# Kernel optimization log

Hardware: AMD Instinct MI355X
Metric: run time of the kernel (lower is better)

## Reference

```python
import jax, jax.numpy as jnp
import numpy as np

B, T, N, D = 32, 12, 325, 64
H = 4           # geo_num_heads == t_num_heads
HD = D // H     # head_dim = 16
M_SP = 32       # spatial frequency modes (min(32, N//2))
M_T = T // 2    # temporal frequency modes (all low modes)
SCALE = HD ** -0.5


def _lin(x, W):
    # torch nn.Linear (no bias): y = x @ W.T, W: [out, in]
    return jnp.einsum('btnd,ed->btne', x, W)


def _spatial(x, Wq, Wk, Wv, weights_Q, sp_modes):
    # FEDformer-style frequency attention over the node axis N
    q, k, v = _lin(x, Wq), _lin(x, Wk), _lin(x, Wv)          # [B,T,N,D]
    prep = lambda y: y.reshape(B, T, N, H, HD).transpose(0, 1, 3, 4, 2)  # [B,T,H,HD,N]
    qn = prep(q) / jnp.linalg.norm(q)   # global Frobenius norm (torch.norm with no dim)
    kn = prep(k) / jnp.linalg.norm(k)
    vn = prep(v)
    # rfft over nodes, gather selected modes (scatter-into-zeros in torch == gather here
    # since target indices are 0..M-1)
    qf = jnp.fft.rfft(qn, axis=-1)[..., sp_modes]            # [B,T,H,HD,M] c64
    kf = jnp.fft.rfft(kn, axis=-1)[..., sp_modes]
    vf = jnp.fft.rfft(vn, axis=-1)[..., sp_modes]
    M = M_SP
    qg = qf.transpose(0, 1, 2, 4, 3)[:, :, :, :, None, :]    # [B,T,H,M,1,HD]
    wq = jnp.broadcast_to(weights_Q.astype(jnp.complex64), (B, T, H, M, M - 1, HD))
    q_cat = jnp.concatenate([qg, wq], axis=4)                # [B,T,H,M,M,HD]
    kg = kf.transpose(0, 1, 2, 4, 3)[:, :, :, None, :, :]    # [B,T,H,1,M,HD]
    att = kg * jnp.conj(q_cat) * SCALE                       # [B,T,H,M,M,HD] c64
    att = jax.nn.softmax(jnp.abs(att), axis=-2).astype(jnp.complex64)
    att = att.transpose(0, 1, 2, 3, 5, 4)                    # [B,T,H,M,HD,M]
    vg = vf[:, :, :, None, :, :]                             # [B,T,H,1,HD,M]
    out = (vg * jnp.conj(att)).mean(axis=3)                  # [B,T,H,HD,M]
    out_ft = jnp.zeros((B, T, H, HD, N // 2 + 1), jnp.complex64).at[..., sp_modes].set(out)
    y = jnp.fft.irfft(out_ft, n=N, axis=-1)                  # [B,T,H,HD,N]
    return y.transpose(0, 1, 4, 2, 3).reshape(B, T, N, D)


def _temporal(x, Wq, Wk, Wv, weights_Q_t, t_modes):
    # frequency attention over the time axis T with causal (tril) mask.
    # NOTE: torch reshapes the [B,T,N,D] buffer directly as [B,N,T,H,HD] (raw view),
    # so we replicate that exact buffer reinterpretation.
    q, k, v = _lin(x, Wq), _lin(x, Wk), _lin(x, Wv)
    prep = lambda y: y.reshape(B, N, T, H, HD).transpose(0, 1, 3, 4, 2)  # [B,N,H,HD,T]
    qn = prep(q); kn = prep(k); vn = prep(v)
    qn = qn / jnp.linalg.norm(qn)
    kn = kn / jnp.linalg.norm(kn)
    qf = jnp.fft.rfft(qn, axis=-1)[..., t_modes]             # [B,N,H,HD,Mt]
    kf = jnp.fft.rfft(kn, axis=-1)[..., t_modes]
    vf = jnp.fft.rfft(vn, axis=-1)[..., t_modes]
    Mt = M_T
    qg = qf.transpose(0, 1, 2, 4, 3)[:, :, :, :, None, :]    # [B,N,H,Mt,1,HD]
    wq = jnp.broadcast_to(weights_Q_t.astype(jnp.complex64), (B, N, H, Mt, Mt - 1, HD))
    q_cat = jnp.concatenate([qg, wq], axis=4)                # [B,N,H,Mt,Mt,HD]
    kg = kf.transpose(0, 1, 2, 4, 3)[:, :, :, :, None, :]    # [B,N,H,Mt,1,HD] (unsqueeze(4) in torch)
    att = kg * jnp.conj(q_cat) * SCALE                       # [B,N,H,Mt,Mt,HD]
    att = att.transpose(0, 1, 2, 5, 3, 4)                    # [B,N,H,HD,Mt,Mt]
    mask = jnp.tril(jnp.ones((Mt, Mt), jnp.float32))
    att = att * mask                                         # zero above diagonal
    attw = jax.nn.softmax(jnp.abs(att), axis=-1).astype(jnp.complex64)
    vg = vf[..., None]                                       # [B,N,H,HD,Mt,1]
    out = (vg * jnp.conj(attw)).mean(axis=-1)                # [B,N,H,HD,Mt]
    out_ft = jnp.zeros((B, N, H, HD, T // 2 + 1), jnp.complex64).at[..., t_modes].set(out)
    y = jnp.fft.irfft(out_ft, n=T, axis=-1)                  # [B,N,H,HD,T]
    return y.transpose(0, 4, 1, 2, 3).reshape(B, T, N, D)


def _gcn(x, adj, W_fc1, W_mlp, b_mlp):
    a = adj / jnp.sum(adj, axis=1, keepdims=True)            # row-normalized
    agg = jnp.einsum('btkd,nk->btnd', x, a)
    h = jnp.einsum('btnd,ed->btne', agg, W_fc1)              # fc1 (no bias)
    return jnp.einsum('btnd,ed->btne', h, W_mlp) + b_mlp     # mlp (bias)


def _forward(x, adj, Wq_geo, Wk_geo, Wv_geo, Wq_t, Wk_t, Wv_t,
             W_fc1, W_mlp, b_mlp, weights_Q, weights_Q_t, sp_modes, t_modes):
    gcn_out = _gcn(x, adj, W_fc1, W_mlp, b_mlp)
    sp_x = _spatial(x, Wq_geo, Wk_geo, Wv_geo, weights_Q, sp_modes)
    te_x = _temporal(x, Wq_t, Wk_t, Wv_t, weights_Q_t, t_modes)
    return gcn_out + sp_x + te_x   # proj_drop is identity (p=0)


def setup_inputs() -> dict:
    key = jax.random.key(0)
    ks = jax.random.split(key, 13)
    w = lambda k, s: jax.random.normal(k, s, dtype=jnp.float32) * 0.05
    rng = np.random.default_rng(0)
    sp_modes = np.sort(rng.permutation(N // 2)[:M_SP]).astype(np.int32)
    t_modes = np.arange(M_T, dtype=np.int32)  # modes_T == T//2 selects all low modes
    return {
        'x': jax.random.normal(ks[0], (B, T, N, D), dtype=jnp.float32),
        'adj': jax.random.uniform(ks[1], (N, N), dtype=jnp.float32),
        'Wq_geo': w(ks[2], (D, D)), 'Wk_geo': w(ks[3], (D, D)), 'Wv_geo': w(ks[4], (D, D)),
        'Wq_t': w(ks[5], (D, D)), 'Wk_t': w(ks[6], (D, D)), 'Wv_t': w(ks[7], (D, D)),
        'W_fc1': w(ks[8], (D, D)), 'W_mlp': w(ks[9], (D, D)), 'b_mlp': w(ks[10], (D,)),
        'weights_Q': jax.random.normal(ks[11], (M_SP, M_SP - 1, HD), dtype=jnp.float32),
        'weights_Q_t': jax.random.normal(ks[12], (M_T, M_T - 1, HD), dtype=jnp.float32),
        'sp_modes': jnp.asarray(sp_modes),
        't_modes': jnp.asarray(t_modes),
    }


def reference(x, adj, Wq_geo, Wk_geo, Wv_geo, Wq_t, Wk_t, Wv_t,
              W_fc1, W_mlp, b_mlp, weights_Q, weights_Q_t, sp_modes, t_modes):
    return _forward(x, adj, Wq_geo, Wk_geo, Wv_geo, Wq_t, Wk_t, Wv_t,
                    W_fc1, W_mlp, b_mlp, weights_Q, weights_Q_t, sp_modes, t_modes)
```

## Files before the change

kernel.cpp:

```cpp
#include <hip/hip_runtime.h>


typedef unsigned short u16;
typedef short short8 __attribute__((ext_vector_type(8)));
typedef float floatx4 __attribute__((ext_vector_type(4)));

__device__ __forceinline__ u16 f2bf(float f) {
  union { float fp; unsigned int u; } v; v.fp = f;
  unsigned int x = v.u;
  x += 0x7FFF + ((x >> 16) & 1);
  return (u16)(x >> 16);
}

constexpr size_t OFF_NORM = 4096;
constexpr size_t OFF_WQA  = 8208;
constexpr size_t OFF_ANB  = 24080;
constexpr size_t OFF_TB   = 81280;
constexpr size_t OFF_T2   = 102080;
constexpr size_t OFF_OFT  = 112480;
constexpr size_t OFF_XCT  = 898912;
constexpr size_t OFF_WBB  = 5224288;
constexpr size_t OFF_WSPB = 5226336;
constexpr size_t OFF_WVTB = 5232480;
constexpr size_t OFF_XA   = 13211488;

__global__ __launch_bounds__(256) void k_prep(const float* __restrict__ x,
                                              const float* __restrict__ Wmlp,
                                              const float* __restrict__ Wfc1,
                                              const float* __restrict__ wQ,
                                              const float* __restrict__ Wq,
                                              const float* __restrict__ Wk,
                                              const float* __restrict__ Wv,
                                              const int* __restrict__ sp_modes,
                                              float* __restrict__ ws) {
  __shared__ float red[256];
  __shared__ __align__(16) u16 XA[128 * 72];
  const int tid = threadIdx.x;
  const int blk = blockIdx.x;
  u16* WBBu = (u16*)(ws + OFF_WBB);
  if (blk >= 22) {
    const int blk2 = blk - 22;
    const int wv = tid >> 6, lane = tid & 63, lc = lane & 15, quad = lane >> 4;
    const size_t base = (size_t)blk2 * 128;
    for (int i = tid; i < 2048; i += 256) {
      const int row = i >> 4, e0 = (i & 15) * 4;
      const float4 v = *(const float4*)(x + (base + row) * 64 + e0);
      u16* dst = &XA[row * 72 + e0];
      dst[0] = f2bf(v.x); dst[1] = f2bf(v.y); dst[2] = f2bf(v.z); dst[3] = f2bf(v.w);
    }
    __syncthreads();
    floatx4 acc[2][8] = {};
#pragma unroll
    for (int kc = 0; kc < 2; ++kc) {
      short8 af[2];
#pragma unroll
      for (int mi = 0; mi < 2; ++mi)
        af[mi] = *(const short8*)&XA[(32 * wv + 16 * mi + lc) * 72 + kc * 32 + quad * 8];
#pragma unroll
      for (int ni = 0; ni < 8; ++ni) {
        const int g = (ni & 3) * 16 + lc;
        const float* src = ((ni < 4) ? Wq : Wk) + (size_t)g * 64 + kc * 32 + quad * 8;
        float v8[8];
        *(float4*)v8 = *(const float4*)src;
        *(float4*)(v8 + 4) = *(const float4*)(src + 4);
        short8 bf_;
#pragma unroll
        for (int u = 0; u < 8; ++u) bf_[u] = (short)f2bf(v8[u]);
#pragma unroll
        for (int mi = 0; mi < 2; ++mi)
          acc[mi][ni] = __builtin_amdgcn_mfma_f32_16x16x32_bf16(af[mi], bf_, acc[mi][ni], 0, 0, 0);
      }
    }
    float sq = 0.f, sk = 0.f;
#pragma unroll
    for (int mi = 0; mi < 2; ++mi)
#pragma unroll
      for (int reg = 0; reg < 4; ++reg) {
#pragma unroll
        for (int ni = 0; ni < 4; ++ni) {
          const float v = acc[mi][ni][reg];
          sq = fmaf(v, v, sq);
        }
#pragma unroll
        for (int ni = 4; ni < 8; ++ni) {
          const float v = acc[mi][ni][reg];
          sk = fmaf(v, v, sk);
        }
      }
    for (int off = 32; off > 0; off >>= 1) {
      sq += __shfl_down(sq, off);
      sk += __shfl_down(sk, off);
    }
    if (lane == 0) { red[wv] = sq; red[8 + wv] = sk; }
    __syncthreads();
    if (tid == 0) {
      const size_t bucket = OFF_NORM + 32 * (size_t)(blk2 & 15);
      atomicAdd(&ws[bucket + 0], red[0] + red[1] + red[2] + red[3]);
      atomicAdd(&ws[bucket + 1], red[8] + red[9] + red[10] + red[11]);
    }
    return;
  }
  if (blk == 0) {
    for (int o = tid; o < 4096; o += 256) {
      int g = o >> 6, dd = o & 63;
      float s = 0.f;
      for (int e = 0; e < 64; ++e)
        s = fmaf(Wmlp[g * 64 + e], Wfc1[e * 64 + dd], s);
      WBBu[o] = f2bf(s);
    }
  } else if (blk < 9) {
    for (int i = (blk - 1) * 256 + tid; i < 15872; i += 2048)
      ws[OFF_WQA + i] = fabsf(wQ[i]);
  } else if (blk < 21) {
    const int j = blk - 9;
    u16* T2B = (u16*)(ws + OFF_T2);
    u16* TB = (u16*)(ws + OFF_TB);
    for (int jj = j; jj < 32; jj += 12) {
      const int f = sp_modes[jj];
      const float wgt = (f == 0) ? 1.f : 2.f;
      const int row_re = 8 * (jj >> 2) + (jj & 3);
      const int row_im = row_re + 4;
      for (int n = tid; n < 352; n += 256) {
        float c = 0.f, s = 0.f;
        if (n < 325) {
          int mm = (f * n) % 325;
          float th = 6.283185307179586f * (float)mm * (1.f / 325.f);
          c = cosf(th);
          s = sinf(th);
        }
        TB[(size_t)row_re * 352 + n] = f2bf(c);
        TB[(size_t)row_im * 352 + n] = f2bf(-s);
        if (n < 325) {
          T2B[(size_t)n * 64 + 2 * jj] = f2bf(wgt * (1.f / 325.f) * c);
          T2B[(size_t)n * 64 + 2 * jj + 1] = f2bf(-wgt * (1.f / 325.f) * s);
        }
      }
    }
  } else {
    u16* WSPBu = (u16*)(ws + OFF_WSPB);
    for (int i = tid; i < 12288; i += 256) {
      const int r = i >> 6, e = i & 63;
      const float* src = (r < 64) ? Wq : (r < 128) ? Wk : Wv;
      WSPBu[i] = f2bf(src[(size_t)(r & 63) * 64 + e]);
    }
  }
}

__global__ __launch_bounds__(256) void k_mega(const float* __restrict__ x,
                                              const float* __restrict__ adj,
                                              const float* __restrict__ Wvt,
                                              float* __restrict__ ws) {
  __shared__ __align__(16) float smem[12800];
  const int tid = threadIdx.x;
  const int blk = blockIdx.x;
  const int lane = tid & 63, wv = tid >> 6;
  const int lc = lane & 15, quad = lane >> 4;

  if (blk < 384) {
    const int bt = blk;
    u16* XBu = (u16*)smem;
    float g_nq = 0.f, g_nk = 0.f;
#pragma unroll
    for (int k2 = 0; k2 < 16; ++k2) {
      const float2 v = *(const float2*)(ws + OFF_NORM + 32 * (size_t)k2);
      g_nq += v.x; g_nk += v.y;
    }

    const u16* TB = (const u16*)(ws + OFF_TB);
    const u16* WSPBu = (const u16*)(ws + OFF_WSPB);
    const float* xb = x + (size_t)bt * 20800;
    const int br = tid & 31, be0 = (tid >> 5) * 8;

    {
      float va[4][8];
#pragma unroll
      for (int g = 0; g < 3; ++g) {
        const int nkc = (g < 2) ? 4 : 3;
#pragma unroll
        for (int u = 0; u < 4; ++u) {
          if (u >= nkc) break;
          const int k0 = (g * 4 + u) * 32;
          if (k0 + br < 325) {
            const float* src = xb + (size_t)(k0 + br) * 64 + be0;
            *(float4*)&va[u][0] = *(const float4*)src;
            *(float4*)&va[u][4] = *(const float4*)(src + 4);
          } else {
#pragma unroll
            for (int w = 0; w < 8; ++w) va[u][w] = 0.f;
          }
        }
#pragma unroll
        for (int u = 0; u < 4; ++u) {
          if (u >= nkc) break;
          const int k0 = (g * 4 + u) * 32;
#pragma unroll
          for (int w = 0; w < 8; ++w)
            XBu[(be0 + w) * 360 + k0 + br] = f2bf(va[u][w]);
        }
      }
    }
    __syncthreads();

    floatx4 accA[4] = {};
#pragma unroll
    for (int kc = 0; kc < 11; ++kc) {
      const short8 af = *(const short8*)&TB[(size_t)(16 * wv + lc) * 352 + kc * 32 + quad * 8];
#pragma unroll
      for (int t = 0; t < 4; ++t) {
        const short8 bf_ = *(const short8*)&XBu[(t * 16 + lc) * 360 + kc * 32 + quad * 8];
        accA[t] = __builtin_amdgcn_mfma_f32_16x16x32_bf16(af, bf_, accA[t], 0, 0, 0);
      }
    }
    __syncthreads();

    u16* xfl2 = XBu;
#pragma unroll
    for (int t = 0; t < 4; ++t)
#pragma unroll
      for (int r = 0; r < 4; ++r)
        xfl2[(t >> 1) * 2560 + (16 * wv + quad * 4 + r) * 40 + (t & 1) * 16 + lc] =
            f2bf(accA[t][r]);
    __syncthreads();

    floatx4 acc2[12] = {};
#pragma unroll
    for (int kc2 = 0; kc2 < 2; ++kc2) {
      const short8 af2 = *(const short8*)&xfl2[kc2 * 2560 + (16 * wv + lc) * 40 + quad * 8];
#pragma unroll
      for (int t = 0; t < 12; ++t) {
        const short8 bf2 = *(const short8*)&WSPBu[(t * 16 + lc) * 64 + kc2 * 32 + quad * 8];
        acc2[t] = __builtin_amdgcn_mfma_f32_16x16x32_bf16(af2, bf2, acc2[t], 0, 0, 0);
      }
    }
    __syncthreads();

    float* sq_q = smem + 2560;
    float* sq_k = smem + 4608;
    float* vfre = smem + 6656;
    float* vfim = smem + 8704;
    float* wbar = smem + 10752;
    for (int i = tid; i < 2048; i += 256) wbar[i] = 0.f;
    {
      const int fb = 8 * wv + ((quad >= 2) ? 4 : 0);
      const int isim = quad & 1;
#pragma unroll
      for (int t = 0; t < 12; ++t) {
        const int mat = t >> 2;
        const int d = (t & 3) * 16 + lc;
#pragma unroll
        for (int r = 0; r < 4; ++r) {
          const float v = acc2[t][r];
          if (mat == 2) {
            if (isim) vfim[(fb + r) * 64 + d] = v;
            else vfre[(fb + r) * 64 + d] = v;
          } else {
            const float s2 = v * v + __shfl_xor(v * v, 16);
            if (!isim) {
              if (mat == 0) sq_q[(fb + r) * 64 + d] = s2;
              else sq_k[(fb + r) * 64 + d] = s2;
            }
          }
        }
      }
    }
    __syncthreads();
    const float inv_nq = rsqrtf(g_nq);
    const float inv_nk = rsqrtf(g_nk);
    for (int i = tid; i < 2048; i += 256)
      sq_k[i] = 0.25f * inv_nk * sqrtf(sq_k[i]);
    __syncthreads();
    {
      const int d = tid & 63, fb2 = tid >> 6, hd = d & 15;
      const float* wqa = ws + OFF_WQA;
      float wacc[32];
#pragma unroll
      for (int j = 0; j < 32; ++j) wacc[j] = 0.f;
      for (int r8 = 0; r8 < 8; ++r8) {
        const int m = fb2 + (r8 << 2);
        const float aq = inv_nq * sqrtf(sq_q[m * 64 + d]);
        float sv[32];
        float mx = -1e30f;
#pragma unroll
        for (int j = 0; j < 32; ++j) {
          const float a = (j == 0) ? aq : wqa[(m * 31 + (j - 1)) * 16 + hd];
          const float s = sq_k[j * 64 + d] * a;
          sv[j] = s;
          mx = fmaxf(mx, s);
        }
        float sum = 0.f;
#pragma unroll
        for (int j = 0; j < 32; ++j) {
          const float ev = __expf(sv[j] - mx);
          sv[j] = ev;
          sum += ev;
        }
        const float sc = 0.03125f / sum;
#pragma unroll
        for (int j = 0; j < 32; ++j) wacc[j] += sv[j] * sc;
      }
#pragma unroll
      for (int j = 0; j < 32; ++j) atomicAdd(&wbar[j * 64 + d], wacc[j]);
    }
    __syncthreads();
    unsigned int* OFTu = (unsigned int*)(ws + OFF_OFT) + (size_t)bt * 2048;
    for (int i2 = tid; i2 < 2048; i2 += 256) {
      const int d = i2 >> 5, j = i2 & 31;
      const float w = wbar[j * 64 + d];
      const unsigned int lo = f2bf(vfre[j * 64 + d] * w);
      const unsigned int hi = f2bf(vfim[j * 64 + d] * w);
      OFTu[i2] = lo | (hi << 16);
    }
  } else if (blk < 1359) {
    const int blk2 = blk - 384;
    u16* XAu = (u16*)smem;
    const size_t base = (size_t)blk2 * 128;
    const u16* WBBu = (const u16*)(ws + OFF_WBB);

    for (int i = tid; i < 2048; i += 256) {
      const int row = i >> 4, e0 = (i & 15) * 4;
      const float4 v = *(const float4*)(x + (base + row) * 64 + e0);
      u16* dst = &XAu[row * 72 + e0];
      dst[0] = f2bf(v.x); dst[1] = f2bf(v.y); dst[2] = f2bf(v.z); dst[3] = f2bf(v.w);
    }
    __syncthreads();

    floatx4 acc[2][4] = {};
#pragma unroll
    for (int kc = 0; kc < 2; ++kc) {
      short8 af[2];
#pragma unroll
      for (int mi = 0; mi < 2; ++mi)
        af[mi] = *(const short8*)&XAu[(32 * wv + 16 * mi + lc) * 72 + kc * 32 + quad * 8];
#pragma unroll
      for (int ni = 0; ni < 4; ++ni) {
        const short8 bf_ = *(const short8*)&WBBu[(ni * 16 + lc) * 64 + kc * 32 + quad * 8];
#pragma unroll
        for (int mi = 0; mi < 2; ++mi)
          acc[mi][ni] = __builtin_amdgcn_mfma_f32_16x16x32_bf16(af[mi], bf_, acc[mi][ni], 0, 0, 0);
      }
    }
    __syncthreads();

    u16* xcT = XAu;
#pragma unroll
    for (int ni = 0; ni < 4; ++ni)
#pragma unroll
      for (int mi = 0; mi < 2; ++mi)
#pragma unroll
        for (int reg = 0; reg < 4; ++reg)
          xcT[(ni * 16 + lc) * 132 + 32 * wv + 16 * mi + quad * 4 + reg] =
              f2bf(acc[mi][ni][reg]);
    __syncthreads();
    u16* XCT = (u16*)(ws + OFF_XCT);
    for (int i = tid; i < 8192; i += 256) {
      const int d = i >> 7, r = i & 127;
      const unsigned int row = (unsigned int)(base + r);
      const unsigned int bt = row / 325u;
      const unsigned int n = row - bt * 325u;
      XCT[(size_t)bt * 22528 + (size_t)d * 352 + n] = xcT[d * 132 + r];
    }
  } else if (blk < 2009) {
    const int idx = (blk - 1359) * 256 + tid;
    if (idx >= 32 * 325 * 16) return;
    const int dq = idx & 15;
    const int n = (idx >> 4) % 325;
    const int b = idx / (16 * 325);
    const float* xp = x + ((size_t)b * 3900 + (size_t)n * 12) * 64 + dq * 4;
    float4 s = make_float4(0.f, 0.f, 0.f, 0.f);
    float sign = 1.f;
    for (int k = 0; k < 12; ++k) {
      const float4 v = *(const float4*)(xp + (size_t)k * 64);
      s.x += sign * v.x; s.y += sign * v.y; s.z += sign * v.z; s.w += sign * v.w;
      sign = -sign;
    }
    *(float4*)(ws + OFF_XA + ((size_t)b * 325 + n) * 64 + dq * 4) = s;
  } else if (blk < 2334) {
    const int n = blk - 2009;
    float* red = smem;
    float p = 0.f;
    for (int k = tid; k < 325; k += 256) p += adj[n * 325 + k];
    red[tid] = p;
    __syncthreads();
    for (int s2 = 128; s2 > 0; s2 >>= 1) {
      if (tid < s2) red[tid] += red[tid + s2];
      __syncthreads();
    }
    const float inv = 1.f / red[0];
    u16* ANB = (u16*)(ws + OFF_ANB);
    for (int k = tid; k < 352; k += 256)
      ANB[(size_t)n * 352 + k] = (k < 325) ? f2bf(adj[n * 325 + k] * inv) : (u16)0;
  } else if (blk < 2430) {
    const int idx = (blk - 2334) * 256 + tid;
    u16* p = (u16*)(ws + OFF_XCT) + (size_t)(idx >> 6) * 22528 + (size_t)(idx & 63) * 352;
    for (int c = 325; c < 352; ++c) p[c] = 0;
  } else {
    u16* WVTBu = (u16*)(ws + OFF_WVTB);
    for (int i = tid; i < 4096; i += 256) WVTBu[i] = f2bf(Wvt[i]);
  }
}

__global__ __launch_bounds__(256) void k_final2(const float* __restrict__ x,
                                                const float* __restrict__ bmlp,
                                                float* __restrict__ ws,
                                                float* __restrict__ out) {
  const int tid = threadIdx.x;
  const int bt = blockIdx.x / 3, mc = blockIdx.x % 3;
  const int m0 = mc * 128;
  const int wave = tid >> 6, lane = tid & 63;
  const int quad = lane >> 4, lc = lane & 15;

  const u16* ANB = (const u16*)(ws + OFF_ANB);
  const u16* T2B = (const u16*)(ws + OFF_T2);
  const u16* XCT = (const u16*)(ws + OFF_XCT) + (size_t)bt * 22528;
  const u16* OFT = (const u16*)(ws + OFF_OFT) + (size_t)bt * 4096;
  const u16* WVTBu = (const u16*)(ws + OFF_WVTB);

  const int b = bt / 12, t = bt - b * 12;
  const float sgn12 = ((t & 1) ? -1.f : 1.f) * (1.f / 12.f);

  floatx4 acc[2][4] = {};

#pragma unroll
  for (int c13 = 0; c13 < 13; ++c13) {
    const bool gcn = (c13 < 11);
    const u16* Asrc = gcn ? ANB : T2B;
    const int astr = gcn ? 352 : 64;
    const int acol = gcn ? c13 * 32 : (c13 - 11) * 32;
    const u16* Bsrc = gcn ? XCT : OFT;
    const int bstr = gcn ? 352 : 64;
    short8 af[2], bf_[4];
#pragma unroll
    for (int mi = 0; mi < 2; ++mi) {
      const int gr = m0 + wave * 32 + mi * 16 + lc;
      short8 a = {};
      if (gr < 325)
        a = *(const short8*)&Asrc[(size_t)gr * astr + acol + quad * 8];
      af[mi] = a;
    }
#pragma unroll
    for (int ni = 0; ni < 4; ++ni)
      bf_[ni] = *(const short8*)&Bsrc[(size_t)(ni * 16 + lc) * bstr + acol + quad * 8];
#pragma unroll
    for (int mi = 0; mi < 2; ++mi)
#pragma unroll
      for (int ni = 0; ni < 4; ++ni)
        acc[mi][ni] = __builtin_amdgcn_mfma_f32_16x16x32_bf16(
            af[mi], bf_[ni], acc[mi][ni], 0, 0, 0);
  }

#pragma unroll
  for (int kc = 0; kc < 2; ++kc) {
    const int k0 = kc * 32 + quad * 8;
    short8 af[2];
#pragma unroll
    for (int mi = 0; mi < 2; ++mi) {
      const int nr = m0 + wave * 32 + mi * 16 + lc;
      short8 a = {};
      if (nr < 325) {
        const float* xp = x + ((size_t)b * 3900 + (size_t)nr * 12 + t) * 64 + k0;
        const float* xap = ws + OFF_XA + ((size_t)b * 325 + nr) * 64 + k0;
        float xv[8], av[8];
        *(float4*)xv = *(const float4*)xp;
        *(float4*)(xv + 4) = *(const float4*)(xp + 4);
        *(float4*)av = *(const float4*)xap;
        *(float4*)(av + 4) = *(const float4*)(xap + 4);
#pragma unroll
        for (int u = 0; u < 8; ++u)
          a[u] = (short)f2bf((xv[u] - sgn12 * av[u]) * (1.f / 6.f));
      }
      af[mi] = a;
    }
#pragma unroll
    for (int ni = 0; ni < 4; ++ni) {
      const short8 bf_ = *(const short8*)&WVTBu[(size_t)(ni * 16 + lc) * 64 + k0];
#pragma unroll
      for (int mi = 0; mi < 2; ++mi)
        acc[mi][ni] = __builtin_amdgcn_mfma_f32_16x16x32_bf16(
            af[mi], bf_, acc[mi][ni], 0, 0, 0);
    }
  }

#pragma unroll
  for (int ni = 0; ni < 4; ++ni) {
    const int d = ni * 16 + lc;
    const float bias = bmlp[d];
#pragma unroll
    for (int mi = 0; mi < 2; ++mi) {
#pragma unroll
      for (int reg = 0; reg < 4; ++reg) {
        const int n = m0 + wave * 32 + mi * 16 + quad * 4 + reg;
        if (n >= 325) continue;
        out[((size_t)bt * 325 + n) * 64 + d] = acc[mi][ni][reg] + bias;
      }
    }
  }
}

extern "C" void kernel_launch(void* const* d_in, const int* in_sizes, int n_in,
                              void* d_out, int out_size, void* d_ws, size_t ws_size,
                              hipStream_t stream) {
  const float* x = (const float*)d_in[0];
  const float* adj = (const float*)d_in[1];
  const float* Wq_g = (const float*)d_in[2];
  const float* Wk_g = (const float*)d_in[3];
  const float* Wv_g = (const float*)d_in[4];
  const float* Wv_t = (const float*)d_in[7];
  const float* Wfc1 = (const float*)d_in[8];
  const float* Wmlp = (const float*)d_in[9];
  const float* bmlp = (const float*)d_in[10];
  const float* wQ = (const float*)d_in[11];
  const int* sp_modes = (const int*)d_in[13];
  float* ws = (float*)d_ws;
  float* out = (float*)d_out;

  (void)in_sizes; (void)n_in; (void)out_size; (void)ws_size;

  hipMemsetAsync(ws + OFF_NORM, 0, 16 * 32 * sizeof(float), stream);
  k_prep<<<997, 256, 0, stream>>>(x, Wmlp, Wfc1, wQ, Wq_g, Wk_g, Wv_g,
                                  sp_modes, ws);
  k_mega<<<2431, 256, 0, stream>>>(x, adj, Wv_t, ws);
  k_final2<<<1152, 256, 0, stream>>>(x, bmlp, ws, out);
}
```

Before: 235.4 us.

## Move global norm reduction into mega kernel with spin-wait counter

Moves the Q/K Frobenius-norm reduction blocks from the prep kernel into the mega kernel. They are placed at the lowest block indices and signal completion through an atomic counter. The spatial blocks compute their FFT projections first and only then spin-wait on the counter before they need the norms. This overlaps the norm pass with other independent work and shortens the prep kernel's critical path. It relies on the earlier blocks being scheduled first to avoid deadlock, and adds spin-polling and atomic overhead.

```diff
diff --git a/kernel.cpp b/kernel.cpp
--- a/kernel.cpp
+++ b/kernel.cpp
@@ -24,8 +24,7 @@
 constexpr size_t OFF_WVTB = 5232480;
 constexpr size_t OFF_XA   = 13211488;
 
-__global__ __launch_bounds__(256) void k_prep(const float* __restrict__ x,
-                                              const float* __restrict__ Wmlp,
+__global__ __launch_bounds__(256) void k_prep(const float* __restrict__ Wmlp,
                                               const float* __restrict__ Wfc1,
                                               const float* __restrict__ wQ,
                                               const float* __restrict__ Wq,
@@ -33,73 +32,9 @@
                                               const float* __restrict__ Wv,
                                               const int* __restrict__ sp_modes,
                                               float* __restrict__ ws) {
-  __shared__ float red[256];
-  __shared__ __align__(16) u16 XA[128 * 72];
   const int tid = threadIdx.x;
   const int blk = blockIdx.x;
   u16* WBBu = (u16*)(ws + OFF_WBB);
-  if (blk >= 22) {
-    const int blk2 = blk - 22;
-    const int wv = tid >> 6, lane = tid & 63, lc = lane & 15, quad = lane >> 4;
-    const size_t base = (size_t)blk2 * 128;
-    for (int i = tid; i < 2048; i += 256) {
-      const int row = i >> 4, e0 = (i & 15) * 4;
-      const float4 v = *(const float4*)(x + (base + row) * 64 + e0);
-      u16* dst = &XA[row * 72 + e0];
-      dst[0] = f2bf(v.x); dst[1] = f2bf(v.y); dst[2] = f2bf(v.z); dst[3] = f2bf(v.w);
-    }
-    __syncthreads();
-    floatx4 acc[2][8] = {};
-#pragma unroll
-    for (int kc = 0; kc < 2; ++kc) {
-      short8 af[2];
-#pragma unroll
-      for (int mi = 0; mi < 2; ++mi)
-        af[mi] = *(const short8*)&XA[(32 * wv + 16 * mi + lc) * 72 + kc * 32 + quad * 8];
-#pragma unroll
-      for (int ni = 0; ni < 8; ++ni) {
-        const int g = (ni & 3) * 16 + lc;
-        const float* src = ((ni < 4) ? Wq : Wk) + (size_t)g * 64 + kc * 32 + quad * 8;
-        float v8[8];
-        *(float4*)v8 = *(const float4*)src;
-        *(float4*)(v8 + 4) = *(const float4*)(src + 4);
-        short8 bf_;
-#pragma unroll
-        for (int u = 0; u < 8; ++u) bf_[u] = (short)f2bf(v8[u]);
-#pragma unroll
-        for (int mi = 0; mi < 2; ++mi)
-          acc[mi][ni] = __builtin_amdgcn_mfma_f32_16x16x32_bf16(af[mi], bf_, acc[mi][ni], 0, 0, 0);
-      }
-    }
-    float sq = 0.f, sk = 0.f;
-#pragma unroll
-    for (int mi = 0; mi < 2; ++mi)
-#pragma unroll
-      for (int reg = 0; reg < 4; ++reg) {
-#pragma unroll
-        for (int ni = 0; ni < 4; ++ni) {
-          const float v = acc[mi][ni][reg];
-          sq = fmaf(v, v, sq);
-        }
-#pragma unroll
-        for (int ni = 4; ni < 8; ++ni) {
-          const float v = acc[mi][ni][reg];
-          sk = fmaf(v, v, sk);
-        }
-      }
-    for (int off = 32; off > 0; off >>= 1) {
-      sq += __shfl_down(sq, off);
-      sk += __shfl_down(sk, off);
-    }
-    if (lane == 0) { red[wv] = sq; red[8 + wv] = sk; }
-    __syncthreads();
-    if (tid == 0) {
-      const size_t bucket = OFF_NORM + 32 * (size_t)(blk2 & 15);
-      atomicAdd(&ws[bucket + 0], red[0] + red[1] + red[2] + red[3]);
-      atomicAdd(&ws[bucket + 1], red[8] + red[9] + red[10] + red[11]);
-    }
-    return;
-  }
   if (blk == 0) {
     for (int o = tid; o < 4096; o += 256) {
       int g = o >> 6, dd = o & 63;
@@ -148,6 +83,8 @@
 
 __global__ __launch_bounds__(256) void k_mega(const float* __restrict__ x,
                                               const float* __restrict__ adj,
+                                              const float* __restrict__ Wq,
+                                              const float* __restrict__ Wk,
                                               const float* __restrict__ Wvt,
                                               float* __restrict__ ws) {
   __shared__ __align__(16) float smem[12800];
@@ -156,15 +93,71 @@
   const int lane = tid & 63, wv = tid >> 6;
   const int lc = lane & 15, quad = lane >> 4;
 
-  if (blk < 384) {
-    const int bt = blk;
+  if (blk < 975) {
+    u16* XAu = (u16*)smem;
+    float* red = smem + 4608;
+    const size_t base = (size_t)blk * 128;
+    for (int i = tid; i < 2048; i += 256) {
+      const int row = i >> 4, e0 = (i & 15) * 4;
+      const float4 v = *(const float4*)(x + (base + row) * 64 + e0);
+      u16* dst = &XAu[row * 72 + e0];
+      dst[0] = f2bf(v.x); dst[1] = f2bf(v.y); dst[2] = f2bf(v.z); dst[3] = f2bf(v.w);
+    }
+    __syncthreads();
+    floatx4 acc[2][8] = {};
+#pragma unroll
+    for (int kc = 0; kc < 2; ++kc) {
+      short8 af[2];
+#pragma unroll
+      for (int mi = 0; mi < 2; ++mi)
+        af[mi] = *(const short8*)&XAu[(32 * wv + 16 * mi + lc) * 72 + kc * 32 + quad * 8];
+#pragma unroll
+      for (int ni = 0; ni < 8; ++ni) {
+        const int g = (ni & 3) * 16 + lc;
+        const float* src = ((ni < 4) ? Wq : Wk) + (size_t)g * 64 + kc * 32 + quad * 8;
+        float v8[8];
+        *(float4*)v8 = *(const float4*)src;
+        *(float4*)(v8 + 4) = *(const float4*)(src + 4);
+        short8 bf_;
+#pragma unroll
+        for (int u = 0; u < 8; ++u) bf_[u] = (short)f2bf(v8[u]);
+#pragma unroll
+        for (int mi = 0; mi < 2; ++mi)
+          acc[mi][ni] = __builtin_amdgcn_mfma_f32_16x16x32_bf16(af[mi], bf_, acc[mi][ni], 0, 0, 0);
+      }
+    }
+    float sq = 0.f, sk = 0.f;
+#pragma unroll
+    for (int mi = 0; mi < 2; ++mi)
+#pragma unroll
+      for (int reg = 0; reg < 4; ++reg) {
+#pragma unroll
+        for (int ni = 0; ni < 4; ++ni) {
+          const float v = acc[mi][ni][reg];
+          sq = fmaf(v, v, sq);
+        }
+#pragma unroll
+        for (int ni = 4; ni < 8; ++ni) {
+          const float v = acc[mi][ni][reg];
+          sk = fmaf(v, v, sk);
+        }
+      }
+    for (int off = 32; off > 0; off >>= 1) {
+      sq += __shfl_down(sq, off);
+      sk += __shfl_down(sk, off);
+    }
+    if (lane == 0) { red[wv] = sq; red[8 + wv] = sk; }
+    __syncthreads();
+    if (tid == 0) {
+      const size_t bucket = OFF_NORM + 32 * (size_t)(blk & 15);
+      atomicAdd(&ws[bucket + 0], red[0] + red[1] + red[2] + red[3]);
+      atomicAdd(&ws[bucket + 1], red[8] + red[9] + red[10] + red[11]);
+      __threadfence();
+      atomicAdd((unsigned int*)&ws[OFF_NORM + 512], 1u);
+    }
+  } else if (blk < 1359) {
+    const int bt = blk - 975;
     u16* XBu = (u16*)smem;
-    float g_nq = 0.f, g_nk = 0.f;
-#pragma unroll
-    for (int k2 = 0; k2 < 16; ++k2) {
-      const float2 v = *(const float2*)(ws + OFF_NORM + 32 * (size_t)k2);
-      g_nq += v.x; g_nk += v.y;
-    }
 
     const u16* TB = (const u16*)(ws + OFF_TB);
     const u16* WSPBu = (const u16*)(ws + OFF_WSPB);
@@ -263,9 +256,22 @@
         }
       }
     }
-    __syncthreads();
-    const float inv_nq = rsqrtf(g_nq);
-    const float inv_nk = rsqrtf(g_nk);
+    if (tid == 0) {
+      unsigned c;
+      do {
+        c = atomicAdd((unsigned int*)&ws[OFF_NORM + 512], 0u);
+        if (c < 975u) __builtin_amdgcn_s_sleep(10);
+      } while (c < 975u);
+      float nq = 0.f, nk = 0.f;
+      for (int k2 = 0; k2 < 16; ++k2) {
+        nq += atomicAdd(&ws[OFF_NORM + 32 * (size_t)k2 + 0], 0.f);
+        nk += atomicAdd(&ws[OFF_NORM + 32 * (size_t)k2 + 1], 0.f);
+      }
+      smem[0] = nq; smem[1] = nk;
+    }
+    __syncthreads();
+    const float inv_nq = rsqrtf(smem[0]);
+    const float inv_nk = rsqrtf(smem[1]);
     for (int i = tid; i < 2048; i += 256)
       sq_k[i] = 0.25f * inv_nk * sqrtf(sq_k[i]);
     __syncthreads();
@@ -310,8 +316,8 @@
       const unsigned int hi = f2bf(vfim[j * 64 + d] * w);
       OFTu[i2] = lo | (hi << 16);
     }
-  } else if (blk < 1359) {
-    const int blk2 = blk - 384;
+  } else if (blk < 2334) {
+    const int blk2 = blk - 1359;
     u16* XAu = (u16*)smem;
     const size_t base = (size_t)blk2 * 128;
     const u16* WBBu = (const u16*)(ws + OFF_WBB);
@@ -359,8 +365,8 @@
       const unsigned int n = row - bt * 325u;
       XCT[(size_t)bt * 22528 + (size_t)d * 352 + n] = xcT[d * 132 + r];
     }
-  } else if (blk < 2009) {
-    const int idx = (blk - 1359) * 256 + tid;
+  } else if (blk < 2984) {
+    const int idx = (blk - 2334) * 256 + tid;
     if (idx >= 32 * 325 * 16) return;
     const int dq = idx & 15;
     const int n = (idx >> 4) % 325;
@@ -374,8 +380,8 @@
       sign = -sign;
     }
     *(float4*)(ws + OFF_XA + ((size_t)b * 325 + n) * 64 + dq * 4) = s;
-  } else if (blk < 2334) {
-    const int n = blk - 2009;
+  } else if (blk < 3309) {
+    const int n = blk - 2984;
     float* red = smem;
     float p = 0.f;
     for (int k = tid; k < 325; k += 256) p += adj[n * 325 + k];
@@ -389,8 +395,8 @@
     u16* ANB = (u16*)(ws + OFF_ANB);
     for (int k = tid; k < 352; k += 256)
       ANB[(size_t)n * 352 + k] = (k < 325) ? f2bf(adj[n * 325 + k] * inv) : (u16)0;
-  } else if (blk < 2430) {
-    const int idx = (blk - 2334) * 256 + tid;
+  } else if (blk < 3405) {
+    const int idx = (blk - 3309) * 256 + tid;
     u16* p = (u16*)(ws + OFF_XCT) + (size_t)(idx >> 6) * 22528 + (size_t)(idx & 63) * 352;
     for (int c = 325; c < 352; ++c) p[c] = 0;
   } else {
@@ -515,9 +521,8 @@
 
   (void)in_sizes; (void)n_in; (void)out_size; (void)ws_size;
 
-  hipMemsetAsync(ws + OFF_NORM, 0, 16 * 32 * sizeof(float), stream);
-  k_prep<<<997, 256, 0, stream>>>(x, Wmlp, Wfc1, wQ, Wq_g, Wk_g, Wv_g,
-                                  sp_modes, ws);
-  k_mega<<<2431, 256, 0, stream>>>(x, adj, Wv_t, ws);
+  hipMemsetAsync(ws + OFF_NORM, 0, 513 * sizeof(float), stream);
+  k_prep<<<22, 256, 0, stream>>>(Wmlp, Wfc1, wQ, Wq_g, Wk_g, Wv_g, sp_modes, ws);
+  k_mega<<<3406, 256, 0, stream>>>(x, adj, Wq_g, Wk_g, Wv_t, ws);
   k_final2<<<1152, 256, 0, stream>>>(x, bmlp, ws, out);
 }
```

New measurement: 300.8 us. +27.8%, slower.
